# Optimization experiments

Measured on AMD Instinct MI355X. Metric: run time of the kernel, lower is better.

The kernel has to match this reference:

```python
import jax, jax.numpy as jnp
import numpy as np

N_MELS = 80
FORMANT_START, FORMANT_END = 10, 50
W_L1, W_DELTA, W_DELTA2, W_SC, W_BAND, FORMANT_W = 1.0, 0.5, 0.25, 0.5, 1.0, 2.0
EPS = 1e-8


def _masked_mean(x, mask):
    # mask broadcasts to x's shape; count = sum of the broadcast mask
    n = jnp.maximum(jnp.sum(jnp.broadcast_to(mask, x.shape)), 1.0)
    return jnp.sum(x * mask) / n


def setup_inputs() -> dict:
    key = jax.random.key(0)
    k1, k2, k3 = jax.random.split(key, 3)
    B, T, D = 64, 4000, N_MELS
    pred_mel = jax.random.normal(k1, (B, T, D), dtype=jnp.float32)
    target_mel = jax.random.normal(k2, (B, T, D), dtype=jnp.float32)
    lengths = jax.random.randint(k3, (B,), T // 2, T + 1)
    mel_mask = (jnp.arange(T)[None, :] < lengths[:, None]).astype(jnp.float32)
    band_weights = jnp.ones((D,), dtype=jnp.float32).at[FORMANT_START:FORMANT_END].set(FORMANT_W)
    return {"pred_mel": pred_mel, "target_mel": target_mel, "mel_mask": mel_mask,
            "band_weights": band_weights}


def reference(pred_mel, target_mel, mel_mask, band_weights):
    mask3 = mel_mask[:, :, None]                      # (B,T,1)

    l1 = jnp.abs(pred_mel - target_mel)               # (B,T,D)
    l1_loss = _masked_mean(l1, mask3)

    # 1st-order deltas
    dp = pred_mel[:, 1:] - pred_mel[:, :-1]
    dt = target_mel[:, 1:] - target_mel[:, :-1]
    dmask = (mel_mask[:, 1:] * mel_mask[:, :-1])[:, :, None]
    delta_loss = _masked_mean(jnp.abs(dp - dt), dmask)

    # 2nd-order deltas
    d2p = dp[:, 1:] - dp[:, :-1]
    d2t = dt[:, 1:] - dt[:, :-1]
    d2mask = (mel_mask[:, 2:] * mel_mask[:, 1:-1] * mel_mask[:, :-2])[:, :, None]
    delta2_loss = _masked_mean(jnp.abs(d2p - d2t), d2mask)

    # spectral convergence
    diff = (pred_mel - target_mel) * mask3
    tgt_m = target_mel * mask3
    n = jnp.maximum(jnp.sum(jnp.broadcast_to(mask3, pred_mel.shape)), 1.0)
    sc_num = jnp.sqrt(jnp.sum(diff * diff) / n)
    sc_den = jnp.maximum(jnp.sqrt(jnp.sum(tgt_m * tgt_m) / n), EPS)
    sc_loss = sc_num / sc_den

    # band-weighted L1
    w = band_weights[None, None, :]
    band_loss = _masked_mean(l1 * w, mask3) / jnp.mean(band_weights)

    # energy (per-frame mean over mel bins)
    e_l1 = jnp.abs(pred_mel.mean(axis=-1) - target_mel.mean(axis=-1))  # (B,T)
    energy_loss = _masked_mean(e_l1, mel_mask)

    return (W_L1 * l1_loss + W_DELTA * delta_loss + W_DELTA2 * delta2_loss
            + W_SC * sc_loss + W_BAND * band_loss + 0.5 * energy_loss)
```

## Files before the change

kernel.cpp:

```cpp
#include <hip/hip_runtime.h>
#include <math.h>

#define D_MELS  80
#define T_DIM   4000
#define F4_ROW  20
#define NQ      10
#define NTHR    256
#define MAXB    1024


__global__ __launch_bounds__(NTHR) void mel_loss_main(
    const float* __restrict__ pred, const float* __restrict__ tgt,
    const float* __restrict__ mask, const float* __restrict__ w,
    float* __restrict__ partial, int BT, int nwaves_total)
{
    const int tid  = threadIdx.x;
    const int lane = tid & 63;
    const int qtr  = lane & 3;
    const int rw   = lane >> 2;
    const int gwave = blockIdx.x * (NTHR / 64) + (tid >> 6);

    const float4* p4 = (const float4*)pred;
    const float4* q4 = (const float4*)tgt;

    float4 wv[5];
    #pragma unroll
    for (int k = 0; k < 5; ++k) wv[k] = ((const float4*)w)[qtr + 4 * k];

    float v_l1 = 0.f, v_band = 0.f, v_diff2 = 0.f, v_tgt2 = 0.f, v_energy = 0.f;
    float v_m = 0.f, v_d = 0.f, v_dm = 0.f, v_d2 = 0.f, v_d2m = 0.f;

    const int row_stride = nwaves_total * 16;

    for (int rbase = gwave * 16; rbase < BT; rbase += row_stride) {
        int r = rbase + rw;
        if (r < BT) {
            int t = r % T_DIM;
            bool has1 = (t >= 1);
            bool has2 = (t >= 2);

            const float4* pr0 = p4 + (size_t)r * F4_ROW + qtr;
            const float4* qr0 = q4 + (size_t)r * F4_ROW + qtr;
            const float4* pr1 = has1 ? pr0 - F4_ROW : pr0;
            const float4* qr1 = has1 ? qr0 - F4_ROW : qr0;
            const float4* pr2 = has2 ? pr0 - 2 * F4_ROW : pr0;
            const float4* qr2 = has2 ? qr0 - 2 * F4_ROW : qr0;

            float mt  = mask[r];
            float mt1 = has1 ? mask[r - 1] : 0.f;
            float mt2 = has2 ? mask[r - 2] : 0.f;

            float l1r = 0.f, bandr = 0.f, sqr = 0.f, t2r = 0.f, er = 0.f;
            float dr = 0.f, d2r = 0.f;

            #pragma unroll
            for (int k = 0; k < 5; ++k) {
                float4 p  = pr0[4 * k];
                float4 qq = qr0[4 * k];
                float4 pa = pr1[4 * k];
                float4 qa = qr1[4 * k];
                float4 pb = pr2[4 * k];
                float4 qb = qr2[4 * k];

                float e0 = p.x - qq.x, e1 = p.y - qq.y,
                      e2 = p.z - qq.z, e3 = p.w - qq.w;
                float f0 = pa.x - qa.x, f1 = pa.y - qa.y,
                      f2 = pa.z - qa.z, f3 = pa.w - qa.w;
                float g0 = pb.x - qb.x, g1 = pb.y - qb.y,
                      g2 = pb.z - qb.z, g3 = pb.w - qb.w;

                float a0 = fabsf(e0), a1 = fabsf(e1),
                      a2 = fabsf(e2), a3 = fabsf(e3);

                l1r   += a0 + a1 + a2 + a3;
                bandr += a0 * wv[k].x + a1 * wv[k].y + a2 * wv[k].z + a3 * wv[k].w;
                sqr   += e0 * e0 + e1 * e1 + e2 * e2 + e3 * e3;
                t2r   += qq.x * qq.x + qq.y * qq.y + qq.z * qq.z + qq.w * qq.w;
                er    += e0 + e1 + e2 + e3;
                dr  += fabsf(e0 - f0) + fabsf(e1 - f1)
                     + fabsf(e2 - f2) + fabsf(e3 - f3);
                d2r += fabsf(e0 - 2.f * f0 + g0) + fabsf(e1 - 2.f * f1 + g1)
                     + fabsf(e2 - 2.f * f2 + g2) + fabsf(e3 - 2.f * f3 + g3);
            }

            float dmv  = mt * mt1;
            float d2mv = dmv * mt2;

            v_l1    += l1r * mt;
            v_band  += bandr * mt;
            v_diff2 += sqr * mt;
            v_tgt2  += t2r * mt;
            v_d     += dr * dmv;
            v_d2    += d2r * d2mv;

            er += __shfl_xor(er, 1, 64);
            er += __shfl_xor(er, 2, 64);
            if (qtr == 0) {
                v_energy += fabsf(er) * mt;
                v_m   += mt;
                v_dm  += dmv;
                v_d2m += d2mv;
            }
        }
    }

    float vals[NQ] = {v_l1, v_band, v_diff2, v_tgt2, v_energy,
                      v_m, v_d, v_dm, v_d2, v_d2m};
    #pragma unroll
    for (int q = 0; q < NQ; ++q) {
        float v = vals[q];
        #pragma unroll
        for (int off = 32; off > 0; off >>= 1)
            v += __shfl_down(v, off, 64);
        vals[q] = v;
    }
    __shared__ float red[NTHR / 64][NQ];
    int wave = tid >> 6;
    if (lane == 0) {
        #pragma unroll
        for (int q = 0; q < NQ; ++q) red[wave][q] = vals[q];
    }
    __syncthreads();
    if (tid < NQ) {
        float s = 0.f;
        #pragma unroll
        for (int wv2 = 0; wv2 < NTHR / 64; ++wv2) s += red[wv2][tid];
        partial[tid * MAXB + blockIdx.x] = s;
    }
}

__global__ __launch_bounds__(640) void mel_loss_finalize(
    const float* __restrict__ partial, const float* __restrict__ w,
    float* __restrict__ out, int nblk)
{
    const int tid = threadIdx.x;
    const int wv  = tid >> 6;
    const int lane = tid & 63;
    __shared__ float fin[NQ];

    float s = 0.f;
    for (int i = lane; i < nblk; i += 64) s += partial[wv * MAXB + i];
    #pragma unroll
    for (int off = 32; off > 0; off >>= 1) s += __shfl_down(s, off, 64);
    if (lane == 0) fin[wv] = s;
    __syncthreads();

    if (tid == 0) {
        float l1s = fin[0], bands = fin[1], diff2 = fin[2], tgt2 = fin[3];
        float energys = fin[4], ms = fin[5], ds = fin[6], dms = fin[7];
        float d2s = fin[8], d2ms = fin[9];

        float wsum = 0.f;
        for (int d = 0; d < D_MELS; ++d) wsum += w[d];
        float wmean = wsum / (float)D_MELS;

        float n1  = fmaxf(ms   * (float)D_MELS, 1.f);
        float nd  = fmaxf(dms  * (float)D_MELS, 1.f);
        float nd2 = fmaxf(d2ms * (float)D_MELS, 1.f);

        float l1_loss     = l1s / n1;
        float delta_loss  = ds / nd;
        float delta2_loss = d2s / nd2;
        float sc_num = sqrtf(diff2 / n1);
        float sc_den = fmaxf(sqrtf(tgt2 / n1), 1e-8f);
        float sc_loss = sc_num / sc_den;
        float band_loss = (bands / n1) / wmean;
        float energy_loss = (energys / (float)D_MELS) / fmaxf(ms, 1.f);

        out[0] = 1.0f * l1_loss + 0.5f * delta_loss + 0.25f * delta2_loss
               + 0.5f * sc_loss + 1.0f * band_loss + 0.5f * energy_loss;
    }
}

extern "C" void kernel_launch(void* const* d_in, const int* in_sizes, int n_in,
                              void* d_out, int out_size, void* d_ws, size_t ws_size,
                              hipStream_t stream) {
    const float* pred = (const float*)d_in[0];
    const float* tgt  = (const float*)d_in[1];
    const float* mask = (const float*)d_in[2];
    const float* w    = (const float*)d_in[3];
    int BT = in_sizes[2];
    float* partial = (float*)d_ws;

    int rows_per_block = (NTHR / 64) * 16;
    int blocks_needed = (BT + rows_per_block - 1) / rows_per_block;
    int grid = blocks_needed < MAXB ? blocks_needed : MAXB;
    int nwaves_total = grid * (NTHR / 64);

    mel_loss_main<<<grid, NTHR, 0, stream>>>(pred, tgt, mask, w, partial, BT, nwaves_total);
    mel_loss_finalize<<<1, 640, 0, stream>>>(partial, w, (float*)d_out, grid);
}
```

Measured before the change: 193.4 us.

## Share neighbor-row differences via wave shuffles instead of reloading previous rows

Each lane now computes only its own row's pred-target difference. It obtains the previous two rows' differences and mask values through __shfl_up from neighboring lane groups, and only the first one or two rows of each 16-row group load their predecessors from memory. This removes the redundant loads of rows t-1 and t-2, which previously tripled global/L2 traffic. Each wave also processes a contiguous 64-row chunk in four unrolled sub-iterations to raise memory-level parallelism. The cost is extra shuffle instructions and more registers, and the boundary handling is subtle.

```diff
diff --git a/kernel.cpp b/kernel.cpp
--- a/kernel.cpp
+++ b/kernel.cpp
@@ -7,12 +7,13 @@
 #define NQ      10
 #define NTHR    256
 #define MAXB    1024
+#define CHUNK   64
 
 
 __global__ __launch_bounds__(NTHR) void mel_loss_main(
     const float* __restrict__ pred, const float* __restrict__ tgt,
     const float* __restrict__ mask, const float* __restrict__ w,
-    float* __restrict__ partial, int BT, int nwaves_total)
+    float* __restrict__ partial, int BT, int total_waves)
 {
     const int tid  = threadIdx.x;
     const int lane = tid & 63;
@@ -30,61 +31,88 @@
     float v_l1 = 0.f, v_band = 0.f, v_diff2 = 0.f, v_tgt2 = 0.f, v_energy = 0.f;
     float v_m = 0.f, v_d = 0.f, v_dm = 0.f, v_d2 = 0.f, v_d2m = 0.f;
 
-    const int row_stride = nwaves_total * 16;
-
-    for (int rbase = gwave * 16; rbase < BT; rbase += row_stride) {
-        int r = rbase + rw;
-        if (r < BT) {
-            int t = r % T_DIM;
+    for (int wbase = gwave * CHUNK; wbase < BT; wbase += total_waves * CHUNK) {
+        #pragma unroll
+        for (int it = 0; it < CHUNK / 16; ++it) {
+            int r = wbase + it * 16 + rw;
+            bool active = (r < BT);
+            int rc = active ? r : (BT - 1);
+            int t = rc % T_DIM;
             bool has1 = (t >= 1);
             bool has2 = (t >= 2);
 
-            const float4* pr0 = p4 + (size_t)r * F4_ROW + qtr;
-            const float4* qr0 = q4 + (size_t)r * F4_ROW + qtr;
-            const float4* pr1 = has1 ? pr0 - F4_ROW : pr0;
-            const float4* qr1 = has1 ? qr0 - F4_ROW : qr0;
-            const float4* pr2 = has2 ? pr0 - 2 * F4_ROW : pr0;
-            const float4* qr2 = has2 ? qr0 - 2 * F4_ROW : qr0;
-
-            float mt  = mask[r];
-            float mt1 = has1 ? mask[r - 1] : 0.f;
-            float mt2 = has2 ? mask[r - 2] : 0.f;
+            const float4* pr = p4 + (size_t)rc * F4_ROW + qtr;
+            const float4* qr = q4 + (size_t)rc * F4_ROW + qtr;
+
+            float4 P[5], Q[5];
+            #pragma unroll
+            for (int k = 0; k < 5; ++k) { P[k] = pr[4 * k]; Q[k] = qr[4 * k]; }
+
+            float4 F[5], G[5];
+            #pragma unroll
+            for (int k = 0; k < 5; ++k) {
+                F[k] = make_float4(0.f, 0.f, 0.f, 0.f);
+                G[k] = make_float4(0.f, 0.f, 0.f, 0.f);
+            }
+            if (rw == 0 && has1 && active) {
+                const float4* pa = pr - F4_ROW;
+                const float4* qa = qr - F4_ROW;
+                #pragma unroll
+                for (int k = 0; k < 5; ++k) {
+                    float4 a = pa[4 * k], b = qa[4 * k];
+                    F[k] = make_float4(a.x - b.x, a.y - b.y, a.z - b.z, a.w - b.w);
+                }
+            }
+            if (rw <= 1 && has2 && active) {
+                const float4* pb = pr - 2 * F4_ROW;
+                const float4* qb = qr - 2 * F4_ROW;
+                #pragma unroll
+                for (int k = 0; k < 5; ++k) {
+                    float4 a = pb[4 * k], b = qb[4 * k];
+                    G[k] = make_float4(a.x - b.x, a.y - b.y, a.z - b.z, a.w - b.w);
+                }
+            }
+
+            float mt = active ? mask[rc] : 0.f;
+            float m1s = __shfl_up(mt, 4, 64);
+            float m2s = __shfl_up(mt, 8, 64);
+            float m1 = has1 ? (rw >= 1 ? m1s : mask[rc - 1]) : 0.f;
+            float m2 = has2 ? (rw >= 2 ? m2s : mask[rc - 2]) : 0.f;
+            if (!active) { m1 = 0.f; m2 = 0.f; }
+
+            float dmv  = mt * m1;
+            float d2mv = dmv * m2;
 
             float l1r = 0.f, bandr = 0.f, sqr = 0.f, t2r = 0.f, er = 0.f;
             float dr = 0.f, d2r = 0.f;
 
             #pragma unroll
             for (int k = 0; k < 5; ++k) {
-                float4 p  = pr0[4 * k];
-                float4 qq = qr0[4 * k];
-                float4 pa = pr1[4 * k];
-                float4 qa = qr1[4 * k];
-                float4 pb = pr2[4 * k];
-                float4 qb = qr2[4 * k];
-
-                float e0 = p.x - qq.x, e1 = p.y - qq.y,
-                      e2 = p.z - qq.z, e3 = p.w - qq.w;
-                float f0 = pa.x - qa.x, f1 = pa.y - qa.y,
-                      f2 = pa.z - qa.z, f3 = pa.w - qa.w;
-                float g0 = pb.x - qb.x, g1 = pb.y - qb.y,
-                      g2 = pb.z - qb.z, g3 = pb.w - qb.w;
-
-                float a0 = fabsf(e0), a1 = fabsf(e1),
-                      a2 = fabsf(e2), a3 = fabsf(e3);
-
+                float4 e = make_float4(P[k].x - Q[k].x, P[k].y - Q[k].y,
+                                       P[k].z - Q[k].z, P[k].w - Q[k].w);
+                float4 s1, s2;
+                s1.x = __shfl_up(e.x, 4, 64); s1.y = __shfl_up(e.y, 4, 64);
+                s1.z = __shfl_up(e.z, 4, 64); s1.w = __shfl_up(e.w, 4, 64);
+                s2.x = __shfl_up(e.x, 8, 64); s2.y = __shfl_up(e.y, 8, 64);
+                s2.z = __shfl_up(e.z, 8, 64); s2.w = __shfl_up(e.w, 8, 64);
+                float4 f, g;
+                f.x = (rw >= 1) ? s1.x : F[k].x; f.y = (rw >= 1) ? s1.y : F[k].y;
+                f.z = (rw >= 1) ? s1.z : F[k].z; f.w = (rw >= 1) ? s1.w : F[k].w;
+                g.x = (rw >= 2) ? s2.x : G[k].x; g.y = (rw >= 2) ? s2.y : G[k].y;
+                g.z = (rw >= 2) ? s2.z : G[k].z; g.w = (rw >= 2) ? s2.w : G[k].w;
+
+                float a0 = fabsf(e.x), a1 = fabsf(e.y), a2 = fabsf(e.z), a3 = fabsf(e.w);
                 l1r   += a0 + a1 + a2 + a3;
                 bandr += a0 * wv[k].x + a1 * wv[k].y + a2 * wv[k].z + a3 * wv[k].w;
-                sqr   += e0 * e0 + e1 * e1 + e2 * e2 + e3 * e3;
-                t2r   += qq.x * qq.x + qq.y * qq.y + qq.z * qq.z + qq.w * qq.w;
-                er    += e0 + e1 + e2 + e3;
-                dr  += fabsf(e0 - f0) + fabsf(e1 - f1)
-                     + fabsf(e2 - f2) + fabsf(e3 - f3);
-                d2r += fabsf(e0 - 2.f * f0 + g0) + fabsf(e1 - 2.f * f1 + g1)
-                     + fabsf(e2 - 2.f * f2 + g2) + fabsf(e3 - 2.f * f3 + g3);
-            }
-
-            float dmv  = mt * mt1;
-            float d2mv = dmv * mt2;
+                sqr   += e.x * e.x + e.y * e.y + e.z * e.z + e.w * e.w;
+                t2r   += Q[k].x * Q[k].x + Q[k].y * Q[k].y
+                       + Q[k].z * Q[k].z + Q[k].w * Q[k].w;
+                er    += e.x + e.y + e.z + e.w;
+                dr    += fabsf(e.x - f.x) + fabsf(e.y - f.y)
+                       + fabsf(e.z - f.z) + fabsf(e.w - f.w);
+                d2r   += fabsf(e.x - 2.f * f.x + g.x) + fabsf(e.y - 2.f * f.y + g.y)
+                       + fabsf(e.z - 2.f * f.z + g.z) + fabsf(e.w - 2.f * f.w + g.w);
+            }
 
             v_l1    += l1r * mt;
             v_band  += bandr * mt;
@@ -182,11 +210,11 @@
     int BT = in_sizes[2];
     float* partial = (float*)d_ws;
 
-    int rows_per_block = (NTHR / 64) * 16;
+    int rows_per_block = (NTHR / 64) * CHUNK;
     int blocks_needed = (BT + rows_per_block - 1) / rows_per_block;
     int grid = blocks_needed < MAXB ? blocks_needed : MAXB;
-    int nwaves_total = grid * (NTHR / 64);
-
-    mel_loss_main<<<grid, NTHR, 0, stream>>>(pred, tgt, mask, w, partial, BT, nwaves_total);
+    int total_waves = grid * (NTHR / 64);
+
+    mel_loss_main<<<grid, NTHR, 0, stream>>>(pred, tgt, mask, w, partial, BT, total_waves);
     mel_loss_finalize<<<1, 640, 0, stream>>>(partial, w, (float*)d_out, grid);
 }
```

Result: slower. 262.1 us (+35.6%).
